# Kernel tuning notes

Hardware: AMD Instinct MI355X
Metric: run time of the kernel (lower is better)

Reference implementation:

```python
import jax, jax.numpy as jnp
import numpy as np

N_NODES = 100000
N_EDGES = 3200000
IN_DIM, HID_DIM, OUT_DIM = 128, 64, 3


def gcn_conv(x, edge_index, W, b):
    """PyG GCNConv: add self-loops, symmetric deg^{-1/2} normalization,
    linear transform then scatter-sum aggregation, plus bias."""
    n = x.shape[0]
    loop = jnp.arange(n, dtype=edge_index.dtype)
    src = jnp.concatenate([edge_index[0], loop])  # [E+N]
    dst = jnp.concatenate([edge_index[1], loop])
    deg = jax.ops.segment_sum(jnp.ones_like(dst, dtype=x.dtype), dst, num_segments=n)
    dinv = jax.lax.rsqrt(jnp.maximum(deg, 1.0))  # deg >= 1 due to self-loops
    norm = dinv[src] * dinv[dst]                 # [E+N]
    h = x @ W                                    # [N, F_out]
    msgs = h[src] * norm[:, None]                # gather + scale
    out = jax.ops.segment_sum(msgs, dst, num_segments=n)
    return out + b


def setup_inputs() -> dict:
    key = jax.random.key(0)
    k1, k2, k3, k4 = jax.random.split(key, 4)
    x = jax.random.normal(k1, (N_NODES, IN_DIM), dtype=jnp.float32)
    edge_index = jax.random.randint(k2, (2, N_EDGES), 0, N_NODES, dtype=jnp.int64)
    W1 = jax.random.normal(k3, (IN_DIM, HID_DIM), dtype=jnp.float32) * (1.0 / np.sqrt(IN_DIM))
    b1 = jnp.zeros((HID_DIM,), dtype=jnp.float32)
    W2 = jax.random.normal(k4, (HID_DIM, OUT_DIM), dtype=jnp.float32) * (1.0 / np.sqrt(HID_DIM))
    b2 = jnp.zeros((OUT_DIM,), dtype=jnp.float32)
    return {"x": x, "edge_index": edge_index, "W1": W1, "b1": b1, "W2": W2, "b2": b2}


def reference(x, edge_index, W1, b1, W2, b2):
    h = gcn_conv(x, edge_index, W1, b1)
    h = jax.nn.relu(h)
    out = gcn_conv(h, edge_index, W2, b2)
    return out
```

## Files before the change

### kernel.cpp

```cpp
#include <hip/hip_runtime.h>
#include <hip/hip_fp16.h>
#include <cstdint>
#include <cstddef>

#define DIM_IN 128
#define DIM_HID 64
#define MS_TILE 16384
#define OVF_CAP 32768
#define BSH 9
#define BINSZ 512
#define MAXNB 512
#define CAPL 20480

typedef int v2i __attribute__((ext_vector_type(2)));

__device__ inline __half2 h2_shfl_xor(__half2 v, int m) {
    int i = __shfl_xor(*reinterpret_cast<int*>(&v), m, 32);
    return *reinterpret_cast<__half2*>(&i);
}
__device__ inline __half2 u2h(unsigned int u) {
    return *reinterpret_cast<__half2*>(&u);
}

__global__ __launch_bounds__(1024) void k_msplit3(const int* __restrict__ eidx,
                                                  int* __restrict__ binCursor,
                                                  unsigned int* __restrict__ binned,
                                                  int* __restrict__ ovfCnt,
                                                  v2i* __restrict__ ovf,
                                                  int E, int NB, int cap) {
    __shared__ int hist[256], base[256];
    __shared__ int stF;
    int t = threadIdx.x;
    if (t == 0) {
        int o = 0;
        for (int j = 1; j < 128; j += 2) o |= eidx[j];
        stF = (o == 0) ? 2 : 1;
    }
    __syncthreads();
    int st = stF;
    int ntiles = (E + MS_TILE - 1) / MS_TILE;

    for (int tile = blockIdx.x; tile < ntiles; tile += gridDim.x) {
        int e0 = tile * MS_TILE;
        int e1 = min(e0 + MS_TILE, E);

        if (t < 256) hist[t] = 0;
        __syncthreads();
        for (int e = e0 + t; e < e1; e += 1024) {
            int d = (st == 2) ? ((const v2i*)eidx)[E + e].x : eidx[E + e];
            atomicAdd(&hist[d >> BSH], 1);
        }
        __syncthreads();
        if (t < NB && hist[t] > 0) base[t] = atomicAdd(&binCursor[t], hist[t]);
        __syncthreads();
        if (t < 256) hist[t] = 0;
        __syncthreads();
        for (int e = e0 + t; e < e1; e += 1024) {
            int s, d;
            if (st == 2) {
                s = ((const v2i*)eidx)[e].x;
                d = ((const v2i*)eidx)[E + e].x;
            } else {
                s = eidx[e];
                d = eidx[E + e];
            }
            int b = d >> BSH;
            int r = atomicAdd(&hist[b], 1);
            int local = base[b] + r;
            if (local < cap) {
                binned[(size_t)b * cap + local] =
                    ((unsigned int)s << BSH) | (unsigned int)(d & (BINSZ - 1));
            } else {
                int o = atomicAdd(ovfCnt, 1);
                if (o < OVF_CAP) ovf[o] = (v2i){s, d};
            }
        }
        __syncthreads();
    }
}

__global__ __launch_bounds__(512) void k_binscan(const int* __restrict__ binCursor,
                                                 int* __restrict__ binBase,
                                                 int NB, int cap) {
    __shared__ int sh[512];
    int t = threadIdx.x;
    int v = (t < NB) ? min(binCursor[t], cap) : 0;
    sh[t] = v;
    __syncthreads();
    for (int d = 1; d < 512; d <<= 1) {
        int add = (t >= d) ? sh[t - d] : 0;
        __syncthreads();
        sh[t] += add;
        __syncthreads();
    }
    if (t < NB) binBase[t] = sh[t] - v;
}

__global__ __launch_bounds__(512) void k_fillA(const unsigned int* __restrict__ binned,
                                               const int* __restrict__ binCursor,
                                               const int* __restrict__ binBase,
                                               int* __restrict__ offsets,
                                               int* __restrict__ cursor,
                                               float* __restrict__ dinv,
                                               int* __restrict__ csr,
                                               int cap, int N) {
    __shared__ int hist[BINSZ], scanS[BINSZ], curL[BINSZ];
    __shared__ unsigned int stage[CAPL];
    int b = blockIdx.x;
    int t = threadIdx.x;
    int g0 = b << BSH;
    int g = g0 + t;
    int n = min(binCursor[b], cap);
    const unsigned int* p = binned + (size_t)b * cap;

    hist[t] = 0;
    __syncthreads();
    for (int i = t; i < n; i += 512)
        atomicAdd(&hist[p[i] & (BINSZ - 1)], 1);
    __syncthreads();
    int h = hist[t];
    scanS[t] = h;
    __syncthreads();
    for (int d = 1; d < 512; d <<= 1) {
        int add = (t >= d) ? scanS[t - d] : 0;
        __syncthreads();
        scanS[t] += add;
        __syncthreads();
    }
    int excl = scanS[t] - h;
    int gbase = binBase[b];
    if (g < N) {
        offsets[g] = gbase + excl;
        dinv[g] = rsqrtf((float)(h + 1));
    }
    if (t == 511) offsets[min(g0 + BINSZ, N)] = gbase + scanS[511];

    curL[t] = excl;
    __syncthreads();
    int nl = min(n, CAPL);
    for (int i = t; i < nl; i += 512) {
        unsigned int w = p[i];
        int pos = atomicAdd(&curL[w & (BINSZ - 1)], 1);
        if (pos < CAPL) stage[pos] = w >> BSH;
    }
    __syncthreads();
    if (g < N) cursor[g] = gbase + curL[t];
    for (int i = t; i < nl; i += 512)
        csr[gbase + i] = (int)stage[i];
    __syncthreads();
    for (int i = CAPL + t; i < n; i += 512) {
        unsigned int w = p[i];
        int pos = atomicAdd(&cursor[g0 + (int)(w & (BINSZ - 1))], 1);
        csr[pos] = (int)(w >> BSH);
    }
}

__global__ void k_ovf(const int* __restrict__ ovfCnt, const v2i* __restrict__ ovf,
                      int* __restrict__ cursor, int* __restrict__ csr) {
    int n = min(*ovfCnt, OVF_CAP);
    for (int i = threadIdx.x; i < n; i += 256) {
        v2i e = ovf[i];
        int pos = atomicAdd(&cursor[e.y], 1);
        csr[pos] = e.x;
    }
}

__global__ __launch_bounds__(256) void k_gemm1t(const float* __restrict__ x,
                                                const float* __restrict__ W,
                                                const float* __restrict__ dinv,
                                                __half2* __restrict__ h1, int N) {
    __shared__ __half xsT[DIM_IN * 64];
    __shared__ float Ws[DIM_IN * DIM_HID];
    int t = threadIdx.x;
    int row0 = blockIdx.x * 64;

#pragma unroll
    for (int i = 0; i < 8; i++)
        ((float4*)Ws)[t + 256 * i] = ((const float4*)W)[t + 256 * i];

#pragma unroll
    for (int i = 0; i < 8; i++) {
        int idx = t * 8 + i;
        int r = idx >> 5;
        int kc = idx & 31;
        int row = row0 + r;
        float4 v = (row < N) ? ((const float4*)(x + (size_t)row * DIM_IN))[kc]
                             : make_float4(0.f, 0.f, 0.f, 0.f);
        xsT[(4 * kc + 0) * 64 + r] = __float2half(v.x);
        xsT[(4 * kc + 1) * 64 + r] = __float2half(v.y);
        xsT[(4 * kc + 2) * 64 + r] = __float2half(v.z);
        xsT[(4 * kc + 3) * 64 + r] = __float2half(v.w);
    }
    __syncthreads();

    int c = t & 15;
    int r = t >> 4;
    float acc[4][4] = {};

#pragma unroll 4
    for (int k = 0; k < DIM_IN; k++) {
        __half2 xh01 = *(const __half2*)&xsT[k * 64 + 4 * r];
        __half2 xh23 = *(const __half2*)&xsT[k * 64 + 4 * r + 2];
        float2 x01 = __half22float2(xh01);
        float2 x23 = __half22float2(xh23);
        float4 wb = *(const float4*)&Ws[k * DIM_HID + 4 * c];
        float xi[4] = {x01.x, x01.y, x23.x, x23.y};
#pragma unroll
        for (int i = 0; i < 4; i++) {
            acc[i][0] = fmaf(xi[i], wb.x, acc[i][0]);
            acc[i][1] = fmaf(xi[i], wb.y, acc[i][1]);
            acc[i][2] = fmaf(xi[i], wb.z, acc[i][2]);
            acc[i][3] = fmaf(xi[i], wb.w, acc[i][3]);
        }
    }

#pragma unroll
    for (int i = 0; i < 4; i++) {
        int row = row0 + 4 * r + i;
        if (row < N) {
            float d = dinv[row];
            h1[(size_t)row * 32 + 2 * c] = __floats2half2_rn(acc[i][0] * d, acc[i][1] * d);
            h1[(size_t)row * 32 + 2 * c + 1] = __floats2half2_rn(acc[i][2] * d, acc[i][3] * d);
        }
    }
}

__global__ __launch_bounds__(256) void k_agg1(const __half2* __restrict__ h1,
                                              const int* __restrict__ csr,
                                              const int* __restrict__ offsets,
                                              const float* __restrict__ dinv,
                                              const float* __restrict__ b1,
                                              const float* __restrict__ W2,
                                              float4* __restrict__ h2, int N) {
    __shared__ float W2s[DIM_HID * 3];
    __shared__ float b1s[DIM_HID];
    int t = threadIdx.x;
    if (t < DIM_HID * 3) W2s[t] = W2[t];
    if (t < DIM_HID) b1s[t] = b1[t];
    __syncthreads();

    int hl = t & 31;
    int slot = hl >> 3;
    int f8 = hl & 7;
    int node = blockIdx.x * 8 + (t >> 5);
    if (node >= N) return;

    const uint4* h1q = (const uint4*)h1;
    float di = dinv[node];
    int beg = offsets[node], end = offsets[node + 1];

    __half2 a0, a1, a2, a3;
    if (slot == 0) {
        uint4 v = h1q[(size_t)node * 8 + f8];
        a0 = u2h(v.x); a1 = u2h(v.y); a2 = u2h(v.z); a3 = u2h(v.w);
    } else {
        a0 = a1 = a2 = a3 = __floats2half2_rn(0.f, 0.f);
    }

    for (int base = beg; base < end; base += 32) {
        int cnt = min(32, end - base);
        int sidx = (hl < cnt) ? csr[base + hl] : 0;
        int iters = (cnt + 3) >> 2;
        for (int j = 0; j < iters; j++) {
            int idx = 4 * j + slot;
            int s = __shfl(sidx, idx, 32);
            if (idx < cnt) {
                uint4 v = h1q[(size_t)s * 8 + f8];
                a0 = __hadd2(a0, u2h(v.x));
                a1 = __hadd2(a1, u2h(v.y));
                a2 = __hadd2(a2, u2h(v.z));
                a3 = __hadd2(a3, u2h(v.w));
            }
        }
    }

    a0 = __hadd2(a0, h2_shfl_xor(a0, 8));  a0 = __hadd2(a0, h2_shfl_xor(a0, 16));
    a1 = __hadd2(a1, h2_shfl_xor(a1, 8));  a1 = __hadd2(a1, h2_shfl_xor(a1, 16));
    a2 = __hadd2(a2, h2_shfl_xor(a2, 8));  a2 = __hadd2(a2, h2_shfl_xor(a2, 16));
    a3 = __hadd2(a3, h2_shfl_xor(a3, 8));  a3 = __hadd2(a3, h2_shfl_xor(a3, 16));

    if (slot == 0) {
        float2 f0 = __half22float2(a0), f1 = __half22float2(a1);
        float2 f2 = __half22float2(a2), f3 = __half22float2(a3);
        float acc[8] = {f0.x, f0.y, f1.x, f1.y, f2.x, f2.y, f3.x, f3.y};
        float v0 = 0.f, v1 = 0.f, v2 = 0.f;
#pragma unroll
        for (int k = 0; k < 8; k++) {
            int f = 8 * f8 + k;
            float gg = fmaxf(fmaf(acc[k], di, b1s[f]), 0.f);
            v0 = fmaf(gg, W2s[f * 3 + 0], v0);
            v1 = fmaf(gg, W2s[f * 3 + 1], v1);
            v2 = fmaf(gg, W2s[f * 3 + 2], v2);
        }
#pragma unroll
        for (int off = 4; off > 0; off >>= 1) {
            v0 += __shfl_xor(v0, off, 8);
            v1 += __shfl_xor(v1, off, 8);
            v2 += __shfl_xor(v2, off, 8);
        }
        if (f8 == 0) h2[node] = make_float4(v0 * di, v1 * di, v2 * di, 0.f);
    }
}

__global__ __launch_bounds__(256) void k_agg2(const float4* __restrict__ h2,
                                              const int* __restrict__ csr,
                                              const int* __restrict__ offsets,
                                              const float* __restrict__ dinv,
                                              const float* __restrict__ b2,
                                              float* __restrict__ out, int N) {
    int t = threadIdx.x;
    int l = t & 7;
    int node = blockIdx.x * 32 + (t >> 3);
    if (node >= N) return;

    float di = dinv[node];
    int beg = offsets[node], end = offsets[node + 1];
    float a0 = 0.f, a1 = 0.f, a2 = 0.f;
    for (int e = beg + l; e < end; e += 8) {
        float4 h = h2[csr[e]];
        a0 += h.x;
        a1 += h.y;
        a2 += h.z;
    }
#pragma unroll
    for (int off = 4; off > 0; off >>= 1) {
        a0 += __shfl_xor(a0, off, 8);
        a1 += __shfl_xor(a1, off, 8);
        a2 += __shfl_xor(a2, off, 8);
    }
    if (l == 0) {
        float4 hs = h2[node];
        out[(size_t)node * 3 + 0] = fmaf(a0 + hs.x, di, b2[0]);
        out[(size_t)node * 3 + 1] = fmaf(a1 + hs.y, di, b2[1]);
        out[(size_t)node * 3 + 2] = fmaf(a2 + hs.z, di, b2[2]);
    }
}

extern "C" void kernel_launch(void* const* d_in, const int* in_sizes, int n_in,
                              void* d_out, int out_size, void* d_ws, size_t ws_size,
                              hipStream_t stream) {
    const float* x = (const float*)d_in[0];
    const int* eidx = (const int*)d_in[1];
    const float* W1 = (const float*)d_in[2];
    const float* b1 = (const float*)d_in[3];
    const float* W2 = (const float*)d_in[4];
    const float* b2 = (const float*)d_in[5];
    float* out = (float*)d_out;

    const int N = in_sizes[0] / DIM_IN;
    const int E = in_sizes[1] / 2;
    const int NB = (N + BINSZ - 1) >> BSH;

    char* w = (char*)d_ws;
    size_t off = 0;
    auto carve = [&](size_t bytes) -> char* {
        char* p = w + off;
        off += (bytes + 255) & ~(size_t)255;
        return p;
    };
    int* offsets = (int*)carve((size_t)(N + 1) * 4);
    int* cursor = (int*)carve((size_t)N * 4);
    float* dinv = (float*)carve((size_t)N * 4);
    int* csr = (int*)carve((size_t)E * 4);
    int* binCursor = (int*)carve(MAXNB * 4);
    int* ovfCnt = (int*)carve(16);
    v2i* ovf = (v2i*)carve((size_t)OVF_CAP * 8);
    int* binBase = (int*)carve(MAXNB * 4);
    float4* h2 = (float4*)carve((size_t)N * 16);

    size_t h1_bytes = (size_t)N * DIM_HID * 2;
    int capDes = E / NB + E / NB / 16 + 256;
    size_t binned_des = (size_t)NB * capDes * 4;
    size_t uni_avail = (ws_size > off + 256) ? (ws_size - off - 256) : h1_bytes;
    size_t uni_bytes = binned_des > h1_bytes ? binned_des : h1_bytes;
    if (uni_bytes > uni_avail) uni_bytes = uni_avail > h1_bytes ? uni_avail : h1_bytes;
    char* uni = carve(uni_bytes);
    unsigned int* binned = (unsigned int*)uni;
    __half2* h1 = (__half2*)uni;
    int cap = (int)(uni_bytes / ((size_t)NB * 4));
    if (cap > capDes) cap = capDes;
    if (cap > CAPL) cap = CAPL;

    (void)hipMemsetAsync(binCursor, 0, MAXNB * 4 + 256, stream);

    int ntiles = (E + MS_TILE - 1) / MS_TILE;
    k_msplit3<<<ntiles, 1024, 0, stream>>>(eidx, binCursor, binned, ovfCnt, ovf,
                                           E, NB, cap);
    k_binscan<<<1, 512, 0, stream>>>(binCursor, binBase, NB, cap);
    k_fillA<<<NB, 512, 0, stream>>>(binned, binCursor, binBase, offsets, cursor,
                                    dinv, csr, cap, N);
    k_ovf<<<1, 256, 0, stream>>>(ovfCnt, ovf, cursor, csr);

    k_gemm1t<<<(N + 63) / 64, 256, 0, stream>>>(x, W1, dinv, h1, N);
    k_agg1<<<(N + 7) / 8, 256, 0, stream>>>(h1, csr, offsets, dinv, b1, W2, h2, N);
    k_agg2<<<(N + 31) / 32, 256, 0, stream>>>(h2, csr, offsets, dinv, b2, out, N);
}
```

Measured before the change: 174.8 us.

## Fold bin scan and overflow kernels into neighbors, unroll agg1 gather loop

Drops the separate bin prefix-scan launch: each fillA block now sums the preceding bins' counts itself with a wavefront reduction. The overflow-edge insertion kernel becomes an extra block appended to the gemm1 launch. This removes two small serialized launches. agg1 also gets a two-way unrolled gather loop with predicated loads and a launch-bounds occupancy hint, which adds register pressure but increases memory-level parallelism.

```diff
diff --git a/kernel.cpp b/kernel.cpp
--- a/kernel.cpp
+++ b/kernel.cpp
@@ -79,33 +79,16 @@
     }
 }
 
-__global__ __launch_bounds__(512) void k_binscan(const int* __restrict__ binCursor,
-                                                 int* __restrict__ binBase,
-                                                 int NB, int cap) {
-    __shared__ int sh[512];
-    int t = threadIdx.x;
-    int v = (t < NB) ? min(binCursor[t], cap) : 0;
-    sh[t] = v;
-    __syncthreads();
-    for (int d = 1; d < 512; d <<= 1) {
-        int add = (t >= d) ? sh[t - d] : 0;
-        __syncthreads();
-        sh[t] += add;
-        __syncthreads();
-    }
-    if (t < NB) binBase[t] = sh[t] - v;
-}
-
 __global__ __launch_bounds__(512) void k_fillA(const unsigned int* __restrict__ binned,
                                                const int* __restrict__ binCursor,
-                                               const int* __restrict__ binBase,
                                                int* __restrict__ offsets,
                                                int* __restrict__ cursor,
                                                float* __restrict__ dinv,
                                                int* __restrict__ csr,
-                                               int cap, int N) {
+                                               int cap, int NB, int N) {
     __shared__ int hist[BINSZ], scanS[BINSZ], curL[BINSZ];
     __shared__ unsigned int stage[CAPL];
+    __shared__ int gbaseS;
     int b = blockIdx.x;
     int t = threadIdx.x;
     int g0 = b << BSH;
@@ -113,6 +96,13 @@
     int n = min(binCursor[b], cap);
     const unsigned int* p = binned + (size_t)b * cap;
 
+    if (t < 64) {
+        int acc = 0;
+        for (int i = t; i < b; i += 64) acc += min(binCursor[i], cap);
+#pragma unroll
+        for (int off = 32; off > 0; off >>= 1) acc += __shfl_xor(acc, off, 64);
+        if (t == 0) gbaseS = acc;
+    }
     hist[t] = 0;
     __syncthreads();
     for (int i = t; i < n; i += 512)
@@ -128,7 +118,7 @@
         __syncthreads();
     }
     int excl = scanS[t] - h;
-    int gbase = binBase[b];
+    int gbase = gbaseS;
     if (g < N) {
         offsets[g] = gbase + excl;
         dinv[g] = rsqrtf((float)(h + 1));
@@ -155,23 +145,27 @@
     }
 }
 
-__global__ void k_ovf(const int* __restrict__ ovfCnt, const v2i* __restrict__ ovf,
-                      int* __restrict__ cursor, int* __restrict__ csr) {
-    int n = min(*ovfCnt, OVF_CAP);
-    for (int i = threadIdx.x; i < n; i += 256) {
-        v2i e = ovf[i];
-        int pos = atomicAdd(&cursor[e.y], 1);
-        csr[pos] = e.x;
-    }
-}
-
 __global__ __launch_bounds__(256) void k_gemm1t(const float* __restrict__ x,
                                                 const float* __restrict__ W,
                                                 const float* __restrict__ dinv,
-                                                __half2* __restrict__ h1, int N) {
+                                                __half2* __restrict__ h1, int N,
+                                                const int* __restrict__ ovfCnt,
+                                                const v2i* __restrict__ ovf,
+                                                int* __restrict__ cursor,
+                                                int* __restrict__ csr) {
+    int t = threadIdx.x;
+    if (blockIdx.x == gridDim.x - 1) {
+        int n = min(*ovfCnt, OVF_CAP);
+        for (int i = t; i < n; i += 256) {
+            v2i e = ovf[i];
+            int pos = atomicAdd(&cursor[e.y], 1);
+            csr[pos] = e.x;
+        }
+        return;
+    }
+
     __shared__ __half xsT[DIM_IN * 64];
     __shared__ float Ws[DIM_IN * DIM_HID];
-    int t = threadIdx.x;
     int row0 = blockIdx.x * 64;
 
 #pragma unroll
@@ -225,13 +219,13 @@
     }
 }
 
-__global__ __launch_bounds__(256) void k_agg1(const __half2* __restrict__ h1,
-                                              const int* __restrict__ csr,
-                                              const int* __restrict__ offsets,
-                                              const float* __restrict__ dinv,
-                                              const float* __restrict__ b1,
-                                              const float* __restrict__ W2,
-                                              float4* __restrict__ h2, int N) {
+__global__ __launch_bounds__(256, 8) void k_agg1(const __half2* __restrict__ h1,
+                                                 const int* __restrict__ csr,
+                                                 const int* __restrict__ offsets,
+                                                 const float* __restrict__ dinv,
+                                                 const float* __restrict__ b1,
+                                                 const float* __restrict__ W2,
+                                                 float4* __restrict__ h2, int N) {
     __shared__ float W2s[DIM_HID * 3];
     __shared__ float b1s[DIM_HID];
     int t = threadIdx.x;
@@ -261,15 +255,27 @@
         int cnt = min(32, end - base);
         int sidx = (hl < cnt) ? csr[base + hl] : 0;
         int iters = (cnt + 3) >> 2;
-        for (int j = 0; j < iters; j++) {
-            int idx = 4 * j + slot;
-            int s = __shfl(sidx, idx, 32);
-            if (idx < cnt) {
-                uint4 v = h1q[(size_t)s * 8 + f8];
-                a0 = __hadd2(a0, u2h(v.x));
-                a1 = __hadd2(a1, u2h(v.y));
-                a2 = __hadd2(a2, u2h(v.z));
-                a3 = __hadd2(a3, u2h(v.w));
+        int j = 0;
+        for (; j + 1 < iters; j += 2) {
+            int i0 = 4 * j + slot;
+            int i1 = i0 + 4;
+            int s0 = __shfl(sidx, i0, 32);
+            int s1 = __shfl(sidx, i1, 32);
+            bool p0 = i0 < cnt, p1 = i1 < cnt;
+            uint4 v0 = p0 ? h1q[(size_t)s0 * 8 + f8] : make_uint4(0, 0, 0, 0);
+            uint4 v1 = p1 ? h1q[(size_t)s1 * 8 + f8] : make_uint4(0, 0, 0, 0);
+            a0 = __hadd2(a0, u2h(v0.x)); a1 = __hadd2(a1, u2h(v0.y));
+            a2 = __hadd2(a2, u2h(v0.z)); a3 = __hadd2(a3, u2h(v0.w));
+            a0 = __hadd2(a0, u2h(v1.x)); a1 = __hadd2(a1, u2h(v1.y));
+            a2 = __hadd2(a2, u2h(v1.z)); a3 = __hadd2(a3, u2h(v1.w));
+        }
+        if (j < iters) {
+            int i0 = 4 * j + slot;
+            int s0 = __shfl(sidx, i0, 32);
+            if (i0 < cnt) {
+                uint4 v = h1q[(size_t)s0 * 8 + f8];
+                a0 = __hadd2(a0, u2h(v.x)); a1 = __hadd2(a1, u2h(v.y));
+                a2 = __hadd2(a2, u2h(v.z)); a3 = __hadd2(a3, u2h(v.w));
             }
         }
     }
@@ -365,7 +371,6 @@
     int* binCursor = (int*)carve(MAXNB * 4);
     int* ovfCnt = (int*)carve(16);
     v2i* ovf = (v2i*)carve((size_t)OVF_CAP * 8);
-    int* binBase = (int*)carve(MAXNB * 4);
     float4* h2 = (float4*)carve((size_t)N * 16);
 
     size_t h1_bytes = (size_t)N * DIM_HID * 2;
@@ -386,12 +391,10 @@
     int ntiles = (E + MS_TILE - 1) / MS_TILE;
     k_msplit3<<<ntiles, 1024, 0, stream>>>(eidx, binCursor, binned, ovfCnt, ovf,
                                            E, NB, cap);
-    k_binscan<<<1, 512, 0, stream>>>(binCursor, binBase, NB, cap);
-    k_fillA<<<NB, 512, 0, stream>>>(binned, binCursor, binBase, offsets, cursor,
-                                    dinv, csr, cap, N);
-    k_ovf<<<1, 256, 0, stream>>>(ovfCnt, ovf, cursor, csr);
-
-    k_gemm1t<<<(N + 63) / 64, 256, 0, stream>>>(x, W1, dinv, h1, N);
+    k_fillA<<<NB, 512, 0, stream>>>(binned, binCursor, offsets, cursor,
+                                    dinv, csr, cap, NB, N);
+    k_gemm1t<<<(N + 63) / 64 + 1, 256, 0, stream>>>(x, W1, dinv, h1, N,
+                                                    ovfCnt, ovf, cursor, csr);
     k_agg1<<<(N + 7) / 8, 256, 0, stream>>>(h1, csr, offsets, dinv, b1, W2, h2, N);
     k_agg2<<<(N + 31) / 32, 256, 0, stream>>>(h2, csr, offsets, dinv, b2, out, N);
 }
```

After: 167.1 us. -4.4%, faster.
